# Performance work log

Hardware: AMD Instinct MI355X
Metric: run time of the kernel (lower is better)

Reference implementation:

```python
import jax, jax.numpy as jnp
import numpy as np

N, E, F, H, C = 50000, 800000, 128, 64, 40
EPS = 1e-12


def _l2norm(x):
    n = jnp.sqrt(jnp.sum(x * x, axis=-1, keepdims=True))
    return x / jnp.maximum(n, EPS)


def _sage_conv(x, edge_index, Wl, bl, Wr, num_nodes):
    # PyG SAGEConv, aggr='mean', normalize=True:
    #   out = lin_l(mean_{j in N(i)} x_j) + lin_r(x_i); out = l2_normalize(out)
    src, dst = edge_index[0], edge_index[1]
    msg = x[src]  # [E, F] gathered neighbor features
    agg = jax.ops.segment_sum(msg, dst, num_segments=num_nodes)
    cnt = jax.ops.segment_sum(jnp.ones((edge_index.shape[1],), x.dtype), dst,
                              num_segments=num_nodes)
    mean = agg / jnp.maximum(cnt, 1.0)[:, None]  # zero-in-degree nodes -> 0
    out = mean @ Wl + bl + x @ Wr
    return _l2norm(out)


def setup_inputs() -> dict:
    key = jax.random.key(0)
    ks = jax.random.split(key, 10)
    s = lambda fan_in: 1.0 / np.sqrt(fan_in)
    x = jax.random.normal(ks[0], (N, F), dtype=jnp.float32)
    edge_index = jax.random.randint(ks[1], (2, E), 0, N, dtype=jnp.int64)
    # conv1: SAGEConv(F -> H); lin_l has bias, lin_r has no bias
    Wl1 = jax.random.uniform(ks[2], (F, H), jnp.float32, -s(F), s(F))
    bl1 = jnp.zeros((H,), jnp.float32)
    Wr1 = jax.random.uniform(ks[3], (F, H), jnp.float32, -s(F), s(F))
    # lin1: Linear(F + H -> H)
    Wlin = jax.random.uniform(ks[4], (F + H, H), jnp.float32, -s(F + H), s(F + H))
    blin = jax.random.uniform(ks[5], (H,), jnp.float32, -s(F + H), s(F + H))
    # conv2: SAGEConv(H -> C)
    Wl2 = jax.random.uniform(ks[6], (H, C), jnp.float32, -s(H), s(H))
    bl2 = jnp.zeros((C,), jnp.float32)
    Wr2 = jax.random.uniform(ks[7], (H, C), jnp.float32, -s(H), s(H))
    return {"x": x, "edge_index": edge_index,
            "Wl1": Wl1, "bl1": bl1, "Wr1": Wr1,
            "Wlin": Wlin, "blin": blin,
            "Wl2": Wl2, "bl2": bl2, "Wr2": Wr2}


def reference(x, edge_index, Wl1, bl1, Wr1, Wlin, blin, Wl2, bl2, Wr2):
    hidden = jax.nn.relu(_sage_conv(x, edge_index, Wl1, bl1, Wr1, N))
    h = jax.nn.relu(jnp.concatenate([x, hidden], axis=1) @ Wlin + blin)
    # dropout is identity in eval mode
    out = _sage_conv(h, edge_index, Wl2, bl2, Wr2, N)
    return out
```

## Files before the change

kernel.cpp:

```cpp
#include <hip/hip_runtime.h>

static constexpr int NN = 50000;
static constexpr int NE = 800000;
static constexpr int F  = 128;
static constexpr int H  = 64;
static constexpr int C  = 40;

static constexpr int NB_BK = 8;
static constexpr int NCH   = 32;
static constexpr int ECH   = NE / NCH;
static constexpr int NBK   = NN / NB_BK;
static constexpr int NCSR  = NB_BK * NCH;
static constexpr int NT64  = (NN + 63) / 64;

typedef __attribute__((ext_vector_type(8))) short bf16x8;
typedef __attribute__((ext_vector_type(8))) unsigned short u16x8;
typedef __attribute__((ext_vector_type(4))) float f32x4;

__device__ inline unsigned short f2bf(float f) {
  unsigned int u = __builtin_bit_cast(unsigned int, f);
  u = (u + 0x7fff + ((u >> 16) & 1)) >> 16;
  return (unsigned short)u;
}
__device__ inline float bf2f(unsigned short u) {
  return __builtin_bit_cast(float, (unsigned int)u << 16);
}



__device__ void hist_body(int bid, const int* __restrict__ ei,
                          int* __restrict__ hist, int* __restrict__ counter) {
  __shared__ int cnt[NBK];
  int i = bid & 7;
  int j = bid >> 3;
  for (int t = threadIdx.x; t < NBK; t += 256) cnt[t] = 0;
  __syncthreads();
  if (bid == 0 && threadIdx.x == 0) *counter = 0;
  int lo = i * NBK;
  const int* dst = ei + NE + j * ECH;
  for (int base = threadIdx.x * 4; base < ECH; base += 256 * 4) {
    int4 d4 = *reinterpret_cast<const int4*>(dst + base);
    if ((unsigned)(d4.x - lo) < (unsigned)NBK) atomicAdd(&cnt[d4.x - lo], 1);
    if ((unsigned)(d4.y - lo) < (unsigned)NBK) atomicAdd(&cnt[d4.y - lo], 1);
    if ((unsigned)(d4.z - lo) < (unsigned)NBK) atomicAdd(&cnt[d4.z - lo], 1);
    if ((unsigned)(d4.w - lo) < (unsigned)NBK) atomicAdd(&cnt[d4.w - lo], 1);
  }
  __syncthreads();
  int* hrow = hist + (size_t)j * NN + lo;
  for (int t = threadIdx.x; t < NBK; t += 256) hrow[t] = cnt[t];
}

__device__ void cvt_body(int bid, const float* __restrict__ x,
                         unsigned short* __restrict__ xb) {
  int id = bid * 256 + threadIdx.x;
  int ns = NT64 * 256;
  for (int i = id; i < NN * F / 4; i += ns) {
    float4 v = reinterpret_cast<const float4*>(x)[i];
    ushort4 o = {f2bf(v.x), f2bf(v.y), f2bf(v.z), f2bf(v.w)};
    reinterpret_cast<ushort4*>(xb)[i] = o;
  }
}

__device__ void scan_body(int bid, int* __restrict__ hist,
                          int* __restrict__ deg, int* __restrict__ start,
                          int* __restrict__ counter) {
  int lane = threadIdx.x & 63;
  int wid  = (bid * 256 + threadIdx.x) >> 6;
  int nchunks = (NN + 63) >> 6;
  if (wid >= nchunks) return;
  int n = (wid << 6) + lane;
  int d = 0;
  if (n < NN) {
    int run = 0;
#pragma unroll
    for (int j = 0; j < NCH; ++j) {
      int v = hist[(size_t)j * NN + n];
      hist[(size_t)j * NN + n] = run;
      run += v;
    }
    d = run;
  }
  int inc = d;
#pragma unroll
  for (int off = 1; off < 64; off <<= 1) {
    int t = __shfl_up(inc, off, 64);
    if (lane >= off) inc += t;
  }
  int total = __shfl(inc, 63, 64);
  int base = 0;
  if (lane == 63) base = atomicAdd(counter, total);
  base = __shfl(base, 63, 64);
  if (n < NN) {
    deg[n]   = d;
    start[n] = base + inc - d;
  }
}

__device__ inline void packW(const float* __restrict__ W, int J, int NT,
                             unsigned short* __restrict__ Wf, int idx) {
  int j  = idx & 7;
  int l  = (idx >> 3) & 63;
  int nt = (idx >> 9) % NT;
  int s  = idx / (512 * NT);
  int k  = s * 32 + (l >> 4) * 8 + j;
  int n  = nt * 16 + (l & 15);
  float v = (n < J) ? W[k * J + n] : 0.f;
  Wf[idx] = f2bf(v);
}

__device__ void prep_body(int bid,
                          const float* __restrict__ Wl1, const float* __restrict__ Wr1,
                          const float* __restrict__ Wlin,
                          const float* __restrict__ Wl2, const float* __restrict__ Wr2,
                          unsigned short* __restrict__ Wf1l, unsigned short* __restrict__ Wf1r,
                          unsigned short* __restrict__ Wflin,
                          unsigned short* __restrict__ Wf2l, unsigned short* __restrict__ Wf2r) {
  int id0 = bid * 256 + threadIdx.x;
  int ns  = 48 * 256;
  for (int i = id0; i < 4 * 4 * 512; i += ns) packW(Wl1, 64, 4, Wf1l, i);
  for (int i = id0; i < 4 * 4 * 512; i += ns) packW(Wr1, 64, 4, Wf1r, i);
  for (int i = id0; i < 6 * 4 * 512; i += ns) packW(Wlin, 64, 4, Wflin, i);
  for (int i = id0; i < 2 * 4 * 512; i += ns) packW(Wl2, 40, 4, Wf2l, i);
  for (int i = id0; i < 2 * 4 * 512; i += ns) packW(Wr2, 40, 4, Wf2r, i);
}

__device__ void fill2_body(int bid, const int* __restrict__ ei,
                           const int* __restrict__ hist,
                           const int* __restrict__ start,
                           int* __restrict__ csr_src) {
  __shared__ int fill[NBK];
  int i = bid & 7;
  int j = bid >> 3;
  int lo = i * NBK;
  const int* hrow = hist + (size_t)j * NN + lo;
  for (int t = threadIdx.x; t < NBK; t += 256) fill[t] = start[lo + t] + hrow[t];
  __syncthreads();
  const int* srcp = ei + j * ECH;
  const int* dstp = ei + NE + j * ECH;
  for (int base = threadIdx.x * 4; base < ECH; base += 256 * 4) {
    int4 s4 = *reinterpret_cast<const int4*>(srcp + base);
    int4 d4 = *reinterpret_cast<const int4*>(dstp + base);
    if ((unsigned)(d4.x - lo) < (unsigned)NBK) { int p = atomicAdd(&fill[d4.x - lo], 1); csr_src[p] = s4.x; }
    if ((unsigned)(d4.y - lo) < (unsigned)NBK) { int p = atomicAdd(&fill[d4.y - lo], 1); csr_src[p] = s4.y; }
    if ((unsigned)(d4.z - lo) < (unsigned)NBK) { int p = atomicAdd(&fill[d4.z - lo], 1); csr_src[p] = s4.z; }
    if ((unsigned)(d4.w - lo) < (unsigned)NBK) { int p = atomicAdd(&fill[d4.w - lo], 1); csr_src[p] = s4.w; }
  }
}


template <int K1, int K2, int JOUT, int NT, int NMAT, bool BIAS, bool RELU, bool OUTBF>
__device__ void mf_body(int bid,
                        const unsigned short* __restrict__ A1,
                        const unsigned short* __restrict__ A2,
                        const unsigned short* __restrict__ Wf0,
                        const unsigned short* __restrict__ Wf1,
                        const float* __restrict__ bias,
                        void* __restrict__ Y0v, void* __restrict__ Y1v) {
  constexpr int K   = K1 + K2;
  constexpr int NKS = K / 32;
  int lane = threadIdx.x & 63;
  int w    = __builtin_amdgcn_readfirstlane(threadIdx.x >> 6);
  int m    = lane & 15;
  int kg   = lane >> 4;
  int n0   = bid * 64;
  int row  = n0 + w * 16 + m;
  int rowc = row < NN ? row : NN - 1;

  f32x4 acc[NMAT][NT];
#pragma unroll
  for (int mt = 0; mt < NMAT; ++mt)
#pragma unroll
    for (int nt = 0; nt < NT; ++nt) acc[mt][nt] = {0.f, 0.f, 0.f, 0.f};

#pragma unroll
  for (int s = 0; s < NKS; ++s) {
    const unsigned short* Ab; int rs, koff;
    if (s * 32 < K1) { Ab = A1; rs = K1; koff = s * 32; }
    else             { Ab = A2; rs = K2; koff = s * 32 - K1; }
    bf16x8 a = *reinterpret_cast<const bf16x8*>(Ab + (size_t)rowc * rs + koff + kg * 8);
#pragma unroll
    for (int mt = 0; mt < NMAT; ++mt) {
      const unsigned short* Wf = (NMAT == 2 && mt) ? Wf1 : Wf0;
#pragma unroll
      for (int nt = 0; nt < NT; ++nt) {
        bf16x8 b = *reinterpret_cast<const bf16x8*>(Wf + (size_t)((s * NT + nt) * 64 + lane) * 8);
        acc[mt][nt] = __builtin_amdgcn_mfma_f32_16x16x32_bf16(a, b, acc[mt][nt], 0, 0, 0);
      }
    }
  }

#pragma unroll
  for (int mt = 0; mt < NMAT; ++mt) {
    void* Yv = (NMAT == 2 && mt) ? Y1v : Y0v;
#pragma unroll
    for (int nt = 0; nt < NT; ++nt) {
      int gc = nt * 16 + m;
      bool cv = gc < JOUT;
      float bb = (BIAS && cv) ? bias[gc] : 0.f;
#pragma unroll
      for (int r = 0; r < 4; ++r) {
        int grow = n0 + w * 16 + kg * 4 + r;
        if (grow < NN && cv) {
          float v = acc[mt][nt][r] + bb;
          if (RELU) v = fmaxf(v, 0.f);
          if (OUTBF) ((unsigned short*)Yv)[(size_t)grow * JOUT + gc] = f2bf(v);
          else       ((float*)Yv)[(size_t)grow * JOUT + gc] = v;
        }
      }
    }
  }
}


__global__ __launch_bounds__(256) void k_p1(const int* __restrict__ ei,
                                            int* __restrict__ hist,
                                            int* __restrict__ counter,
                                            const float* __restrict__ x,
                                            unsigned short* __restrict__ xb) {
  if (blockIdx.x < NCSR) hist_body(blockIdx.x, ei, hist, counter);
  else                   cvt_body(blockIdx.x - NCSR, x, xb);
}

__global__ __launch_bounds__(256) void k_p2(int* __restrict__ hist,
                                            int* __restrict__ deg,
                                            int* __restrict__ start,
                                            int* __restrict__ counter,
                                            const float* Wl1, const float* Wr1,
                                            const float* Wlin,
                                            const float* Wl2, const float* Wr2,
                                            unsigned short* Wf1l, unsigned short* Wf1r,
                                            unsigned short* Wflin,
                                            unsigned short* Wf2l, unsigned short* Wf2r) {
  if (blockIdx.x < 196) scan_body(blockIdx.x, hist, deg, start, counter);
  else prep_body(blockIdx.x - 196, Wl1, Wr1, Wlin, Wl2, Wr2,
                 Wf1l, Wf1r, Wflin, Wf2l, Wf2r);
}

__global__ __launch_bounds__(256) void k_p3(const int* __restrict__ ei,
                                            const int* __restrict__ hist,
                                            const int* __restrict__ start,
                                            int* __restrict__ csr_src,
                                            const unsigned short* __restrict__ xb,
                                            const unsigned short* __restrict__ Wf1l,
                                            const unsigned short* __restrict__ Wf1r,
                                            unsigned short* __restrict__ p1b,
                                            unsigned short* __restrict__ q1b) {
  if (blockIdx.x < NCSR) fill2_body(blockIdx.x, ei, hist, start, csr_src);
  else mf_body<F, 0, H, 4, 2, false, false, true>(blockIdx.x - NCSR, xb, nullptr,
                                                  Wf1l, Wf1r, nullptr, p1b, q1b);
}


__global__ __launch_bounds__(256) void k_lin2(const unsigned short* __restrict__ xb,
                                              const unsigned short* __restrict__ hiddenb,
                                              const unsigned short* __restrict__ Wflin,
                                              const float* __restrict__ blin,
                                              const unsigned short* __restrict__ Wf2l,
                                              const unsigned short* __restrict__ Wf2r,
                                              unsigned short* __restrict__ p2b,
                                              unsigned short* __restrict__ q2b) {
  constexpr int ST2 = 72;
  __shared__ __align__(16) unsigned short hls[4][16][ST2];
  int lane = threadIdx.x & 63;
  int w    = __builtin_amdgcn_readfirstlane(threadIdx.x >> 6);
  int m    = lane & 15;
  int kg   = lane >> 4;
  int n0   = blockIdx.x * 64;
  int row  = n0 + w * 16 + m;
  int rowc = row < NN ? row : NN - 1;

  f32x4 acc[4];
#pragma unroll
  for (int nt = 0; nt < 4; ++nt) acc[nt] = {0.f, 0.f, 0.f, 0.f};
#pragma unroll
  for (int s = 0; s < 6; ++s) {
    const unsigned short* Ab; int rs, koff;
    if (s < 4) { Ab = xb;      rs = F; koff = s * 32; }
    else       { Ab = hiddenb; rs = H; koff = s * 32 - F; }
    bf16x8 a = *reinterpret_cast<const bf16x8*>(Ab + (size_t)rowc * rs + koff + kg * 8);
#pragma unroll
    for (int nt = 0; nt < 4; ++nt) {
      bf16x8 b = *reinterpret_cast<const bf16x8*>(Wflin + (size_t)((s * 4 + nt) * 64 + lane) * 8);
      acc[nt] = __builtin_amdgcn_mfma_f32_16x16x32_bf16(a, b, acc[nt], 0, 0, 0);
    }
  }
#pragma unroll
  for (int nt = 0; nt < 4; ++nt) {
    int gc = nt * 16 + m;
    float bb = blin[gc];
#pragma unroll
    for (int r = 0; r < 4; ++r) {
      float v = fmaxf(acc[nt][r] + bb, 0.f);
      hls[w][kg * 4 + r][gc] = f2bf(v);
    }
  }

  f32x4 acc2[2][3];
#pragma unroll
  for (int mt = 0; mt < 2; ++mt)
#pragma unroll
    for (int nt = 0; nt < 3; ++nt) acc2[mt][nt] = {0.f, 0.f, 0.f, 0.f};
#pragma unroll
  for (int s = 0; s < 2; ++s) {
    bf16x8 a = *reinterpret_cast<const bf16x8*>(&hls[w][m][s * 32 + kg * 8]);
#pragma unroll
    for (int mt = 0; mt < 2; ++mt) {
      const unsigned short* Wf = mt ? Wf2r : Wf2l;
#pragma unroll
      for (int nt = 0; nt < 3; ++nt) {
        bf16x8 b = *reinterpret_cast<const bf16x8*>(Wf + (size_t)((s * 4 + nt) * 64 + lane) * 8);
        acc2[mt][nt] = __builtin_amdgcn_mfma_f32_16x16x32_bf16(a, b, acc2[mt][nt], 0, 0, 0);
      }
    }
  }
#pragma unroll
  for (int mt = 0; mt < 2; ++mt) {
    unsigned short* Yv = mt ? q2b : p2b;
#pragma unroll
    for (int nt = 0; nt < 3; ++nt) {
      int gc = nt * 16 + m;
      if (gc < C) {
#pragma unroll
        for (int r = 0; r < 4; ++r) {
          int grow = n0 + w * 16 + kg * 4 + r;
          if (grow < NN) Yv[(size_t)grow * C + gc] = f2bf(acc2[mt][nt][r]);
        }
      }
    }
  }
}


template <int JCR, bool RELU, bool OUTBF>
__global__ __launch_bounds__(256) void k_aggv(const unsigned short* __restrict__ p,
                                              const unsigned short* __restrict__ q,
                                              const float* __restrict__ bl,
                                              const int* __restrict__ deg,
                                              const int* __restrict__ start,
                                              const int* __restrict__ csr_src,
                                              void* __restrict__ outp) {
  constexpr int ST = (JCR == 64) ? 64 : 40;
  int lane = threadIdx.x & 63;
  int e = lane >> 3, c = lane & 7;
  int co = (c * 8 <= ST - 8) ? c * 8 : ST - 8;
  int wid = (blockIdx.x * blockDim.x + threadIdx.x) >> 6;
  int nw  = (gridDim.x * blockDim.x) >> 6;

  float blv[8];
#pragma unroll
  for (int j = 0; j < 8; ++j) {
    int f = c * 8 + j;
    blv[j] = (f < JCR) ? bl[f] : 0.f;
  }

  for (int node = wid; node < NN; node += nw) {
    int d  = __builtin_amdgcn_readfirstlane(deg[node]);
    int st = __builtin_amdgcn_readfirstlane(start[node]);
    float a0[8], a1[8];
#pragma unroll
    for (int j = 0; j < 8; ++j) { a0[j] = 0.f; a1[j] = 0.f; }
    int r = 0;
    for (; r + 16 <= d; r += 16) {
      int i0 = csr_src[st + r + e];
      int i1 = csr_src[st + r + 8 + e];
      u16x8 v0 = *reinterpret_cast<const u16x8*>(p + (size_t)i0 * ST + co);
      u16x8 v1 = *reinterpret_cast<const u16x8*>(p + (size_t)i1 * ST + co);
#pragma unroll
      for (int j = 0; j < 8; ++j) { a0[j] += bf2f(v0[j]); a1[j] += bf2f(v1[j]); }
    }
    if (r + 8 <= d) {
      int i0 = csr_src[st + r + e];
      u16x8 v0 = *reinterpret_cast<const u16x8*>(p + (size_t)i0 * ST + co);
#pragma unroll
      for (int j = 0; j < 8; ++j) a0[j] += bf2f(v0[j]);
      r += 8;
    }
    int rem = d - r;
    if (rem > 0) {
      int ec = e < rem ? e : rem - 1;
      int i0 = csr_src[st + r + ec];
      u16x8 v0 = *reinterpret_cast<const u16x8*>(p + (size_t)i0 * ST + co);
      if (e < rem) {
#pragma unroll
        for (int j = 0; j < 8; ++j) a0[j] += bf2f(v0[j]);
      }
    }
#pragma unroll
    for (int j = 0; j < 8; ++j) a0[j] += a1[j];
#pragma unroll
    for (int ms = 8; ms <= 32; ms <<= 1)
#pragma unroll
      for (int j = 0; j < 8; ++j) a0[j] += __shfl_xor(a0[j], ms, 64);

    float inv = 1.f / fmaxf((float)d, 1.f);
    u16x8 qv = *reinterpret_cast<const u16x8*>(q + (size_t)node * ST + co);
    float v[8];
    float ss = 0.f;
#pragma unroll
    for (int j = 0; j < 8; ++j) {
      int f = c * 8 + j;
      float t = a0[j] * inv + blv[j] + bf2f(qv[j]);
      if (f >= JCR) t = 0.f;
      v[j] = t;
      ss += t * t;
    }
#pragma unroll
    for (int ms = 1; ms <= 4; ms <<= 1) ss += __shfl_xor(ss, ms, 64);
    float rn = 1.f / fmaxf(sqrtf(ss), 1e-12f);

    if (e == 0 && c * 8 < JCR) {
      if (OUTBF) {
        u16x8 o;
#pragma unroll
        for (int j = 0; j < 8; ++j) {
          float t = v[j] * rn;
          if (RELU) t = fmaxf(t, 0.f);
          o[j] = f2bf(t);
        }
        *reinterpret_cast<u16x8*>((unsigned short*)outp + (size_t)node * JCR + c * 8) = o;
      } else {
        float* op = (float*)outp + (size_t)node * JCR + c * 8;
#pragma unroll
        for (int j = 0; j < 8; j += 4) {
          float4 o = {v[j] * rn, v[j + 1] * rn, v[j + 2] * rn, v[j + 3] * rn};
          if (RELU) {
            o.x = fmaxf(o.x, 0.f); o.y = fmaxf(o.y, 0.f);
            o.z = fmaxf(o.z, 0.f); o.w = fmaxf(o.w, 0.f);
          }
          *reinterpret_cast<float4*>(op + j) = o;
        }
      }
    }
  }
}


static inline size_t align256(size_t x) { return (x + 255) & ~(size_t)255; }

extern "C" void kernel_launch(void* const* d_in, const int* in_sizes, int n_in,
                              void* d_out, int out_size, void* d_ws, size_t ws_size,
                              hipStream_t stream) {
  const float* x    = (const float*)d_in[0];
  const int*   ei   = (const int*)d_in[1];
  const float* Wl1  = (const float*)d_in[2];
  const float* bl1  = (const float*)d_in[3];
  const float* Wr1  = (const float*)d_in[4];
  const float* Wlin = (const float*)d_in[5];
  const float* blin = (const float*)d_in[6];
  const float* Wl2  = (const float*)d_in[7];
  const float* bl2  = (const float*)d_in[8];
  const float* Wr2  = (const float*)d_in[9];
  float* out = (float*)d_out;

  char* w = (char*)d_ws;
  size_t off = 0;
  int* deg     = (int*)(w + off); off += align256((size_t)NN * 4);
  int* start   = (int*)(w + off); off += align256((size_t)NN * 4);
  int* counter = (int*)(w + off); off += 256;
  int* csr_src = (int*)(w + off); off += align256((size_t)NE * 4);
  int* hist    = (int*)(w + off); off += align256((size_t)NCH * NN * 4);
  unsigned short* xb      = (unsigned short*)(w + off); off += align256((size_t)NN * F * 2);
  unsigned short* hiddenb = (unsigned short*)(w + off); off += align256((size_t)NN * H * 2);
  unsigned short* p1b = (unsigned short*)(w + off); off += align256((size_t)NN * 64 * 2);
  unsigned short* q1b = (unsigned short*)(w + off); off += align256((size_t)NN * 64 * 2);
  unsigned short* p2b = (unsigned short*)(w + off); off += align256((size_t)NN * 40 * 2 + 256);
  unsigned short* q2b = (unsigned short*)(w + off); off += align256((size_t)NN * 40 * 2 + 256);
  unsigned short* Wf1l  = (unsigned short*)(w + off); off += align256(4 * 4 * 512 * 2);
  unsigned short* Wf1r  = (unsigned short*)(w + off); off += align256(4 * 4 * 512 * 2);
  unsigned short* Wflin = (unsigned short*)(w + off); off += align256(6 * 4 * 512 * 2);
  unsigned short* Wf2l  = (unsigned short*)(w + off); off += align256(2 * 4 * 512 * 2);
  unsigned short* Wf2r  = (unsigned short*)(w + off); off += align256(2 * 4 * 512 * 2);

  const int T = 256;

  k_p1<<<NCSR + NT64, T, 0, stream>>>(ei, hist, counter, x, xb);
  k_p2<<<244, T, 0, stream>>>(hist, deg, start, counter,
                              Wl1, Wr1, Wlin, Wl2, Wr2,
                              Wf1l, Wf1r, Wflin, Wf2l, Wf2r);
  k_p3<<<NCSR + NT64, T, 0, stream>>>(ei, hist, start, csr_src,
                                      xb, Wf1l, Wf1r, p1b, q1b);
  k_aggv<H, true, true><<<2048, T, 0, stream>>>(p1b, q1b, bl1, deg, start, csr_src, hiddenb);
  k_lin2<<<NT64, T, 0, stream>>>(xb, hiddenb, Wflin, blin, Wf2l, Wf2r, p2b, q2b);
  k_aggv<C, false, false><<<2048, T, 0, stream>>>(p2b, q2b, bl2, deg, start, csr_src, out);
}
```

Measured before the change: 199.3 us.

## Fuse layer-1 neighbor aggregation into lin/conv2 projection kernel via shared memory

Merges the first SAGE aggregation (mean of projected neighbor features, bias, self term, L2 norm, ReLU) into the kernel that computes the lin1 layer and the conv2 projections. The hidden activations are kept in shared memory per 64-node tile instead of being written to and read back from global memory, and one kernel launch is removed. In exchange, the aggregation now runs with only NT64 blocks (782) of one wave per 16 nodes, processed serially per node, rather than the 2048-block grid-stride aggregation kernel. This may reduce parallelism and latency hiding for the irregular gathers.

```diff
diff --git a/kernel.cpp b/kernel.cpp
--- a/kernel.cpp
+++ b/kernel.cpp
@@ -251,21 +251,105 @@
 }
 
 
-__global__ __launch_bounds__(256) void k_lin2(const unsigned short* __restrict__ xb,
-                                              const unsigned short* __restrict__ hiddenb,
-                                              const unsigned short* __restrict__ Wflin,
-                                              const float* __restrict__ blin,
-                                              const unsigned short* __restrict__ Wf2l,
-                                              const unsigned short* __restrict__ Wf2r,
-                                              unsigned short* __restrict__ p2b,
-                                              unsigned short* __restrict__ q2b) {
-  constexpr int ST2 = 72;
-  __shared__ __align__(16) unsigned short hls[4][16][ST2];
+__global__ __launch_bounds__(256) void k_agl(const unsigned short* __restrict__ p1,
+                                             const unsigned short* __restrict__ q1,
+                                             const float* __restrict__ bl1,
+                                             const int* __restrict__ deg,
+                                             const int* __restrict__ start,
+                                             const int* __restrict__ csr_src,
+                                             const unsigned short* __restrict__ xb,
+                                             const unsigned short* __restrict__ Wflin,
+                                             const float* __restrict__ blin,
+                                             const unsigned short* __restrict__ Wf2l,
+                                             const unsigned short* __restrict__ Wf2r,
+                                             unsigned short* __restrict__ p2b,
+                                             unsigned short* __restrict__ q2b) {
+  constexpr int ST = 64;
+  constexpr int SH = 72;
+  __shared__ __align__(16) unsigned short hid[4][16][SH];
+  __shared__ __align__(16) unsigned short hls[4][16][SH];
   int lane = threadIdx.x & 63;
   int w    = __builtin_amdgcn_readfirstlane(threadIdx.x >> 6);
+  int n0   = blockIdx.x * 64;
+
+  {
+    int e = lane >> 3, c = lane & 7;
+    float blv[8];
+#pragma unroll
+    for (int j = 0; j < 8; ++j) blv[j] = bl1[c * 8 + j];
+
+    for (int k = 0; k < 16; ++k) {
+      int node = n0 + w * 16 + k;
+      if (node >= NN) {
+        if (e == 0) {
+          u16x8 z = {0, 0, 0, 0, 0, 0, 0, 0};
+          *reinterpret_cast<u16x8*>(&hid[w][k][c * 8]) = z;
+        }
+        continue;
+      }
+      int d  = __builtin_amdgcn_readfirstlane(deg[node]);
+      int st = __builtin_amdgcn_readfirstlane(start[node]);
+      float a0[8], a1[8];
+#pragma unroll
+      for (int j = 0; j < 8; ++j) { a0[j] = 0.f; a1[j] = 0.f; }
+      int r = 0;
+      for (; r + 16 <= d; r += 16) {
+        int i0 = csr_src[st + r + e];
+        int i1 = csr_src[st + r + 8 + e];
+        u16x8 v0 = *reinterpret_cast<const u16x8*>(p1 + (size_t)i0 * ST + c * 8);
+        u16x8 v1 = *reinterpret_cast<const u16x8*>(p1 + (size_t)i1 * ST + c * 8);
+#pragma unroll
+        for (int j = 0; j < 8; ++j) { a0[j] += bf2f(v0[j]); a1[j] += bf2f(v1[j]); }
+      }
+      if (r + 8 <= d) {
+        int i0 = csr_src[st + r + e];
+        u16x8 v0 = *reinterpret_cast<const u16x8*>(p1 + (size_t)i0 * ST + c * 8);
+#pragma unroll
+        for (int j = 0; j < 8; ++j) a0[j] += bf2f(v0[j]);
+        r += 8;
+      }
+      int rem = d - r;
+      if (rem > 0) {
+        int ec = e < rem ? e : rem - 1;
+        int i0 = csr_src[st + r + ec];
+        u16x8 v0 = *reinterpret_cast<const u16x8*>(p1 + (size_t)i0 * ST + c * 8);
+        if (e < rem) {
+#pragma unroll
+          for (int j = 0; j < 8; ++j) a0[j] += bf2f(v0[j]);
+        }
+      }
+#pragma unroll
+      for (int j = 0; j < 8; ++j) a0[j] += a1[j];
+#pragma unroll
+      for (int ms = 8; ms <= 32; ms <<= 1)
+#pragma unroll
+        for (int j = 0; j < 8; ++j) a0[j] += __shfl_xor(a0[j], ms, 64);
+
+      float inv = 1.f / fmaxf((float)d, 1.f);
+      u16x8 qv = *reinterpret_cast<const u16x8*>(q1 + (size_t)node * ST + c * 8);
+      float v[8];
+      float ss = 0.f;
+#pragma unroll
+      for (int j = 0; j < 8; ++j) {
+        float t = a0[j] * inv + blv[j] + bf2f(qv[j]);
+        v[j] = t;
+        ss += t * t;
+      }
+#pragma unroll
+      for (int ms = 1; ms <= 4; ms <<= 1) ss += __shfl_xor(ss, ms, 64);
+      float rn = 1.f / fmaxf(sqrtf(ss), 1e-12f);
+
+      if (e == 0) {
+        u16x8 o;
+#pragma unroll
+        for (int j = 0; j < 8; ++j) o[j] = f2bf(fmaxf(v[j] * rn, 0.f));
+        *reinterpret_cast<u16x8*>(&hid[w][k][c * 8]) = o;
+      }
+    }
+  }
+
   int m    = lane & 15;
   int kg   = lane >> 4;
-  int n0   = blockIdx.x * 64;
   int row  = n0 + w * 16 + m;
   int rowc = row < NN ? row : NN - 1;
 
@@ -274,10 +358,9 @@
   for (int nt = 0; nt < 4; ++nt) acc[nt] = {0.f, 0.f, 0.f, 0.f};
 #pragma unroll
   for (int s = 0; s < 6; ++s) {
-    const unsigned short* Ab; int rs, koff;
-    if (s < 4) { Ab = xb;      rs = F; koff = s * 32; }
-    else       { Ab = hiddenb; rs = H; koff = s * 32 - F; }
-    bf16x8 a = *reinterpret_cast<const bf16x8*>(Ab + (size_t)rowc * rs + koff + kg * 8);
+    bf16x8 a;
+    if (s < 4) a = *reinterpret_cast<const bf16x8*>(xb + (size_t)rowc * F + s * 32 + kg * 8);
+    else       a = *reinterpret_cast<const bf16x8*>(&hid[w][m][(s - 4) * 32 + kg * 8]);
 #pragma unroll
     for (int nt = 0; nt < 4; ++nt) {
       bf16x8 b = *reinterpret_cast<const bf16x8*>(Wflin + (size_t)((s * 4 + nt) * 64 + lane) * 8);
@@ -459,8 +542,7 @@
   int* counter = (int*)(w + off); off += 256;
   int* csr_src = (int*)(w + off); off += align256((size_t)NE * 4);
   int* hist    = (int*)(w + off); off += align256((size_t)NCH * NN * 4);
-  unsigned short* xb      = (unsigned short*)(w + off); off += align256((size_t)NN * F * 2);
-  unsigned short* hiddenb = (unsigned short*)(w + off); off += align256((size_t)NN * H * 2);
+  unsigned short* xb  = (unsigned short*)(w + off); off += align256((size_t)NN * F * 2);
   unsigned short* p1b = (unsigned short*)(w + off); off += align256((size_t)NN * 64 * 2);
   unsigned short* q1b = (unsigned short*)(w + off); off += align256((size_t)NN * 64 * 2);
   unsigned short* p2b = (unsigned short*)(w + off); off += align256((size_t)NN * 40 * 2 + 256);
@@ -479,7 +561,7 @@
                               Wf1l, Wf1r, Wflin, Wf2l, Wf2r);
   k_p3<<<NCSR + NT64, T, 0, stream>>>(ei, hist, start, csr_src,
                                       xb, Wf1l, Wf1r, p1b, q1b);
-  k_aggv<H, true, true><<<2048, T, 0, stream>>>(p1b, q1b, bl1, deg, start, csr_src, hiddenb);
-  k_lin2<<<NT64, T, 0, stream>>>(xb, hiddenb, Wflin, blin, Wf2l, Wf2r, p2b, q2b);
+  k_agl<<<NT64, T, 0, stream>>>(p1b, q1b, bl1, deg, start, csr_src,
+                                xb, Wflin, blin, Wf2l, Wf2r, p2b, q2b);
   k_aggv<C, false, false><<<2048, T, 0, stream>>>(p2b, q2b, bl2, deg, start, csr_src, out);
 }
```

Result: slower. 207.6 us (+4.2%).
